# Kernel optimization log

Hardware: AMD Instinct MI355X
Metric: run time of the kernel (lower is better)

## Reference

```python
import jax, jax.numpy as jnp
import numpy as np

N, D = 262144, 256
MARGIN = 0.75


def setup_inputs() -> dict:
    key = jax.random.key(0)
    k1, k2 = jax.random.split(key)
    feature_results = jax.random.normal(k1, (N, D), dtype=jnp.float32)
    target_var = jax.random.uniform(k2, (N,), dtype=jnp.float32)
    return {"feature_results": feature_results, "target_var": target_var}


def reference(feature_results, target_var):
    t = target_var
    # 4 engagement-level masks, [4, N]
    masks = jnp.stack([
        t <= 0.1,
        (t > 0.3) & (t <= 0.4),
        (t > 0.6) & (t <= 0.7),
        (t > 0.8) & (t <= 1.1),
    ]).astype(feature_results.dtype)
    counts = masks.sum(axis=1)                      # [4]
    sums = masks @ feature_results                  # [4, D] masked group sums
    # mean if the group is non-empty, else keep zeros (matches the torch code)
    means = jnp.where(counts[:, None] > 0, sums / jnp.maximum(counts, 1.0)[:, None], 0.0)

    def dist(i, j):
        return jnp.linalg.norm(means[i] - means[j])

    d12, d13, d14 = dist(0, 1), dist(0, 2), dist(0, 3)
    d23, d24, d34 = dist(1, 2), dist(1, 3), dist(2, 3)
    m = MARGIN
    loss = (jax.nn.relu(d12 - d13 + m) + jax.nn.relu(d12 - d14 + 2 * m)
            + jax.nn.relu(d23 - d24 + m) + jax.nn.relu(d23 - d14 + 2 * m)
            + jax.nn.relu(d34 - d24 + m) + jax.nn.relu(d34 - d14 + 2 * m))
    return loss
```

## Files before the change

kernel.cpp:

```cpp
#include <hip/hip_runtime.h>
#include <math.h>

#define D 256
#define COPY_FLOATS 1028
#define NCOPIES_MAX 32
#define GRID_BLOCKS 1024

__global__ __launch_bounds__(256) void group_partial(
    const float* __restrict__ F, const float* __restrict__ T,
    float* __restrict__ ws, int nRows, int ncopies)
{
    __shared__ float lsum[4][4][D];
    __shared__ float lcnt[4][4];

    const int tid  = threadIdx.x;
    const int lane = tid & 63;
    const int wav  = tid >> 6;
    const long long waveId = (long long)blockIdx.x * 4 + wav;
    const long long nWaves = (long long)gridDim.x * 4;

    float4 a0 = {0.f,0.f,0.f,0.f}, a1 = a0, a2 = a0, a3 = a0;
    float c0 = 0.f, c1 = 0.f, c2 = 0.f, c3 = 0.f;

    for (long long base = waveId * 64; base < (long long)nRows;
         base += nWaves * 64) {
        const long long r = base + lane;
        const float t = (r < (long long)nRows) ? T[r] : 2.0f;

        const unsigned long long m0 = __ballot(t <= 0.1f);
        const unsigned long long m1 = __ballot(t > 0.3f && t <= 0.4f);
        const unsigned long long m2 = __ballot(t > 0.6f && t <= 0.7f);
        const unsigned long long m3 = __ballot(t > 0.8f && t <= 1.1f);

        c0 += (float)__popcll(m0);
        c1 += (float)__popcll(m1);
        c2 += (float)__popcll(m2);
        c3 += (float)__popcll(m3);

        const float* Fb = F + (size_t)base * D + (size_t)lane * 4;
        unsigned long long mAll = m0 | m1 | m2 | m3;

        auto addRow = [&](int jj, const float4& v) {
            if ((m0 >> jj) & 1ull) {
                a0.x += v.x; a0.y += v.y; a0.z += v.z; a0.w += v.w;
            } else if ((m1 >> jj) & 1ull) {
                a1.x += v.x; a1.y += v.y; a1.z += v.z; a1.w += v.w;
            } else if ((m2 >> jj) & 1ull) {
                a2.x += v.x; a2.y += v.y; a2.z += v.z; a2.w += v.w;
            } else {
                a3.x += v.x; a3.y += v.y; a3.z += v.z; a3.w += v.w;
            }
        };

        while (__popcll(mAll) >= 4) {
            const int j0 = __ffsll(mAll) - 1; mAll &= mAll - 1;
            const int j1 = __ffsll(mAll) - 1; mAll &= mAll - 1;
            const int j2 = __ffsll(mAll) - 1; mAll &= mAll - 1;
            const int j3 = __ffsll(mAll) - 1; mAll &= mAll - 1;
            const float4 v0 = *reinterpret_cast<const float4*>(Fb + (size_t)j0 * D);
            const float4 v1 = *reinterpret_cast<const float4*>(Fb + (size_t)j1 * D);
            const float4 v2 = *reinterpret_cast<const float4*>(Fb + (size_t)j2 * D);
            const float4 v3 = *reinterpret_cast<const float4*>(Fb + (size_t)j3 * D);
            addRow(j0, v0); addRow(j1, v1); addRow(j2, v2); addRow(j3, v3);
        }
        while (mAll) {
            const int j0 = __ffsll(mAll) - 1; mAll &= mAll - 1;
            const float4 v0 = *reinterpret_cast<const float4*>(Fb + (size_t)j0 * D);
            addRow(j0, v0);
        }
    }

    *reinterpret_cast<float4*>(&lsum[wav][0][lane * 4]) = a0;
    *reinterpret_cast<float4*>(&lsum[wav][1][lane * 4]) = a1;
    *reinterpret_cast<float4*>(&lsum[wav][2][lane * 4]) = a2;
    *reinterpret_cast<float4*>(&lsum[wav][3][lane * 4]) = a3;
    if (lane == 0) {
        lcnt[wav][0] = c0; lcnt[wav][1] = c1; lcnt[wav][2] = c2; lcnt[wav][3] = c3;
    }
    __syncthreads();

    float* dst = ws + (size_t)(blockIdx.x % ncopies) * COPY_FLOATS;
#pragma unroll
    for (int g = 0; g < 4; ++g) {
        const float s = lsum[0][g][tid] + lsum[1][g][tid]
                      + lsum[2][g][tid] + lsum[3][g][tid];
        atomicAdd(dst + g * D + tid, s);
    }
    if (tid < 4) {
        const float c = lcnt[0][tid] + lcnt[1][tid] + lcnt[2][tid] + lcnt[3][tid];
        atomicAdd(dst + 4 * D + tid, c);
    }
}

__global__ __launch_bounds__(256) void finalize(
    const float* __restrict__ ws, int ncopies, float* __restrict__ out)
{
    const int tid  = threadIdx.x;
    const int lane = tid & 63;
    const int wav  = tid >> 6;

    float s[4] = {0.f,0.f,0.f,0.f};
    float c[4] = {0.f,0.f,0.f,0.f};
#pragma unroll 4
    for (int cp = 0; cp < ncopies; ++cp) {
        const float* w = ws + (size_t)cp * COPY_FLOATS;
#pragma unroll
        for (int g = 0; g < 4; ++g) {
            s[g] += w[g * D + tid];
            c[g] += w[4 * D + g];
        }
    }

    float m[4];
#pragma unroll
    for (int g = 0; g < 4; ++g)
        m[g] = (c[g] > 0.f) ? s[g] / fmaxf(c[g], 1.f) : 0.f;

    float p[6];
    p[0] = (m[0]-m[1]) * (m[0]-m[1]);
    p[1] = (m[0]-m[2]) * (m[0]-m[2]);
    p[2] = (m[0]-m[3]) * (m[0]-m[3]);
    p[3] = (m[1]-m[2]) * (m[1]-m[2]);
    p[4] = (m[1]-m[3]) * (m[1]-m[3]);
    p[5] = (m[2]-m[3]) * (m[2]-m[3]);

    __shared__ float red[6][4];
#pragma unroll
    for (int k = 0; k < 6; ++k) {
        float v = p[k];
#pragma unroll
        for (int off = 32; off >= 1; off >>= 1)
            v += __shfl_down(v, off, 64);
        if (lane == 0) red[k][wav] = v;
    }
    __syncthreads();

    if (tid == 0) {
        float d[6];
#pragma unroll
        for (int k = 0; k < 6; ++k)
            d[k] = sqrtf(red[k][0] + red[k][1] + red[k][2] + red[k][3]);
        const float d12 = d[0], d13 = d[1], d14 = d[2];
        const float d23 = d[3], d24 = d[4], d34 = d[5];
        const float M = 0.75f;
        const float loss =
              fmaxf(d12 - d13 + M, 0.f)       + fmaxf(d12 - d14 + 2.f * M, 0.f)
            + fmaxf(d23 - d24 + M, 0.f)       + fmaxf(d23 - d14 + 2.f * M, 0.f)
            + fmaxf(d34 - d24 + M, 0.f)       + fmaxf(d34 - d14 + 2.f * M, 0.f);
        out[0] = loss;
    }
}

extern "C" void kernel_launch(void* const* d_in, const int* in_sizes, int n_in,
                              void* d_out, int out_size, void* d_ws, size_t ws_size,
                              hipStream_t stream) {
    const float* F = (const float*)d_in[0];
    const float* T = (const float*)d_in[1];
    float* out = (float*)d_out;
    const int nRows = in_sizes[1];

    int ncopies = (int)(ws_size / (COPY_FLOATS * sizeof(float)));
    if (ncopies > NCOPIES_MAX) ncopies = NCOPIES_MAX;
    if (ncopies < 1) ncopies = 1;

    hipMemsetAsync(d_ws, 0, (size_t)ncopies * COPY_FLOATS * sizeof(float), stream);

    group_partial<<<GRID_BLOCKS, 256, 0, stream>>>(F, T, (float*)d_ws, nRows, ncopies);
    finalize<<<1, 256, 0, stream>>>((const float*)d_ws, ncopies, out);
}
```

Baseline: 45.34 us.

## Fuse finalize into partial-sum kernel via last-block counter and deepen load batching

Merges the separate finalize launch into the reduction kernel. Each block bumps a global counter after its atomics, and the last block to arrive computes the means, distances and loss. This removes one kernel launch and its gap. It also adds an 8-row batched gather loop ahead of the existing 4-row loop, so more loads are in flight per wave, and sets a min-blocks hint in launch bounds. The cost is a counter atomic and fence per block, a serial tail in the last block, and possible register pressure from the wider batch.

```diff
diff --git a/kernel.cpp b/kernel.cpp
--- a/kernel.cpp
+++ b/kernel.cpp
@@ -6,9 +6,10 @@
 #define NCOPIES_MAX 32
 #define GRID_BLOCKS 1024
 
-__global__ __launch_bounds__(256) void group_partial(
+__global__ __launch_bounds__(256, 4) void rank_loss_fused(
     const float* __restrict__ F, const float* __restrict__ T,
-    float* __restrict__ ws, int nRows, int ncopies)
+    float* __restrict__ ws, unsigned* __restrict__ counter,
+    float* __restrict__ out, int nRows, int ncopies)
 {
     __shared__ float lsum[4][4][D];
     __shared__ float lcnt[4][4];
@@ -52,6 +53,26 @@
             }
         };
 
+        while (__popcll(mAll) >= 8) {
+            const int j0 = __ffsll(mAll) - 1; mAll &= mAll - 1;
+            const int j1 = __ffsll(mAll) - 1; mAll &= mAll - 1;
+            const int j2 = __ffsll(mAll) - 1; mAll &= mAll - 1;
+            const int j3 = __ffsll(mAll) - 1; mAll &= mAll - 1;
+            const int j4 = __ffsll(mAll) - 1; mAll &= mAll - 1;
+            const int j5 = __ffsll(mAll) - 1; mAll &= mAll - 1;
+            const int j6 = __ffsll(mAll) - 1; mAll &= mAll - 1;
+            const int j7 = __ffsll(mAll) - 1; mAll &= mAll - 1;
+            const float4 v0 = *reinterpret_cast<const float4*>(Fb + (size_t)j0 * D);
+            const float4 v1 = *reinterpret_cast<const float4*>(Fb + (size_t)j1 * D);
+            const float4 v2 = *reinterpret_cast<const float4*>(Fb + (size_t)j2 * D);
+            const float4 v3 = *reinterpret_cast<const float4*>(Fb + (size_t)j3 * D);
+            const float4 v4 = *reinterpret_cast<const float4*>(Fb + (size_t)j4 * D);
+            const float4 v5 = *reinterpret_cast<const float4*>(Fb + (size_t)j5 * D);
+            const float4 v6 = *reinterpret_cast<const float4*>(Fb + (size_t)j6 * D);
+            const float4 v7 = *reinterpret_cast<const float4*>(Fb + (size_t)j7 * D);
+            addRow(j0, v0); addRow(j1, v1); addRow(j2, v2); addRow(j3, v3);
+            addRow(j4, v4); addRow(j5, v5); addRow(j6, v6); addRow(j7, v7);
+        }
         while (__popcll(mAll) >= 4) {
             const int j0 = __ffsll(mAll) - 1; mAll &= mAll - 1;
             const int j1 = __ffsll(mAll) - 1; mAll &= mAll - 1;
@@ -90,31 +111,35 @@
         const float c = lcnt[0][tid] + lcnt[1][tid] + lcnt[2][tid] + lcnt[3][tid];
         atomicAdd(dst + 4 * D + tid, c);
     }
-}
 
-__global__ __launch_bounds__(256) void finalize(
-    const float* __restrict__ ws, int ncopies, float* __restrict__ out)
-{
-    const int tid  = threadIdx.x;
-    const int lane = tid & 63;
-    const int wav  = tid >> 6;
+    asm volatile("s_waitcnt vmcnt(0)" ::: "memory");
+    __syncthreads();
+
+    __shared__ int isLast;
+    if (tid == 0) {
+        const unsigned old = atomicAdd(counter, 1u);
+        isLast = (old == (unsigned)(gridDim.x - 1)) ? 1 : 0;
+    }
+    __syncthreads();
+    if (!isLast) return;
+
+    __threadfence();
 
     float s[4] = {0.f,0.f,0.f,0.f};
-    float c[4] = {0.f,0.f,0.f,0.f};
-#pragma unroll 4
+    float cc[4] = {0.f,0.f,0.f,0.f};
     for (int cp = 0; cp < ncopies; ++cp) {
         const float* w = ws + (size_t)cp * COPY_FLOATS;
 #pragma unroll
         for (int g = 0; g < 4; ++g) {
-            s[g] += w[g * D + tid];
-            c[g] += w[4 * D + g];
+            s[g]  += w[g * D + tid];
+            cc[g] += w[4 * D + g];
         }
     }
 
     float m[4];
 #pragma unroll
     for (int g = 0; g < 4; ++g)
-        m[g] = (c[g] > 0.f) ? s[g] / fmaxf(c[g], 1.f) : 0.f;
+        m[g] = (cc[g] > 0.f) ? s[g] / fmaxf(cc[g], 1.f) : 0.f;
 
     float p[6];
     p[0] = (m[0]-m[1]) * (m[0]-m[1]);
@@ -159,12 +184,16 @@
     float* out = (float*)d_out;
     const int nRows = in_sizes[1];
 
-    int ncopies = (int)(ws_size / (COPY_FLOATS * sizeof(float)));
+    int ncopies = (int)((ws_size - 64) / (COPY_FLOATS * sizeof(float)));
     if (ncopies > NCOPIES_MAX) ncopies = NCOPIES_MAX;
     if (ncopies < 1) ncopies = 1;
+    const size_t copies_bytes = (size_t)ncopies * COPY_FLOATS * sizeof(float);
 
-    hipMemsetAsync(d_ws, 0, (size_t)ncopies * COPY_FLOATS * sizeof(float), stream);
+    float* ws = (float*)d_ws;
+    unsigned* counter = (unsigned*)((char*)d_ws + copies_bytes);
 
-    group_partial<<<GRID_BLOCKS, 256, 0, stream>>>(F, T, (float*)d_ws, nRows, ncopies);
-    finalize<<<1, 256, 0, stream>>>((const float*)d_ws, ncopies, out);
+    hipMemsetAsync(d_ws, 0, copies_bytes + 64, stream);
+
+    rank_loss_fused<<<GRID_BLOCKS, 256, 0, stream>>>(
+        F, T, ws, counter, out, nRows, ncopies);
 }
```

Result: slower. 79.88 us (+76.2%).
